# Kernel tuning notes

Measured on AMD Instinct MI355X. Metric: run time of the kernel, lower is better.

## Reference

```python
import jax, jax.numpy as jnp
import numpy as np

R = 2048      # reservoir_size
I = 32        # input_size
O = 32        # output_size
T = 8192      # number of timesteps
SPECTRAL_RADIUS = 0.9


def setup_inputs() -> dict:
    key = jax.random.key(0)
    k1, k2, k3, k4 = jax.random.split(key, 4)
    X = jax.random.normal(k1, (T, I), dtype=jnp.float32)
    # W_in ~ U(-1, 1) as in the torch module
    W_in = jax.random.uniform(k2, (R, I), dtype=jnp.float32, minval=-1.0, maxval=1.0)
    # W_res: random sign-flipped matrix rescaled to target spectral radius.
    # For an iid Gaussian matrix the spectral radius is ~sqrt(R)*std, so
    # scaling by SPECTRAL_RADIUS/sqrt(R) reproduces the rescaling step.
    W_res = jax.random.normal(k3, (R, R), dtype=jnp.float32) * (SPECTRAL_RADIUS / np.sqrt(R))
    W_res = W_res.astype(jnp.float32)
    # W_out: readout over concat([state, input]) -> [O, R + I]
    W_out = jax.random.normal(k4, (O, R + I), dtype=jnp.float32) * 0.02
    state0 = jnp.zeros((R,), dtype=jnp.float32)
    return {"X": X, "W_in": W_in, "W_res": W_res, "W_out": W_out, "state0": state0}


def reference(X, W_in, W_res, W_out, state0):
    """ESN.predict: sequential tanh reservoir recurrence + linear readout.

    state_{t+1} = tanh(W_in @ x_t + W_res @ state_t)
    pred_t      = W_out @ concat([state_{t+1}, x_t])
    Loop runs over the first T-1 inputs (matches `range(X.shape[0]-1)`),
    and since output_size == input_size the torch code returns the T-1
    predictions (initial zero column dropped).
    """
    def step(state, x):  # state: [R], x: [I]
        new_state = jnp.tanh(W_in @ x + W_res @ state)
        pred = W_out @ jnp.concatenate([new_state, x])  # [O]
        return new_state, pred

    _, preds = jax.lax.scan(step, state0, X[:-1])
    return preds  # [T-1, O]
```

## Files before the change

### kernel.cpp

```cpp
#include <hip/hip_runtime.h>
#include <hip/hip_fp16.h>
#include <math.h>


#define R_    2048
#define I_    32
#define O_    32
#define NSTEP 8191
#define G_    256
#define BLK   256
#define TB    4
#define CAPP  (1u << 24)

typedef unsigned int u32;
typedef unsigned long long u64;

__device__ __forceinline__ float tanh_fast(float u) {
    float e = __expf(2.f * u);
    return 1.f - __fdividef(2.f, e + 1.f);
}
__device__ __forceinline__ u32 pkh(float v, u32 tag) {
    return (tag << 16) | (u32)__half_as_ushort(__float2half(v));
}
__device__ __forceinline__ u64 ald(const u64* p) {
    return __hip_atomic_load(p, __ATOMIC_RELAXED, __HIP_MEMORY_SCOPE_AGENT);
}
__device__ __forceinline__ float h2f(u32 b) {
    return __half2float(__ushort_as_half((unsigned short)(b & 0xFFFFu)));
}


__global__ __launch_bounds__(256) void esn_readout(const u32* __restrict__ states,
                                                   const float* __restrict__ W_out,
                                                   const float* __restrict__ X,
                                                   float* __restrict__ out)
{
    __shared__ float s_arr[TB][R_];
    const int t0  = blockIdx.x * TB;
    const int tid = threadIdx.x;
    #pragma unroll
    for (int i = 0; i < TB; ++i) {
        const int t = t0 + i;
        if (t < NSTEP) {
            const u64* p64 = (const u64*)(states + (size_t)(t + 1) * R_);
            #pragma unroll
            for (int q = 0; q < 4; ++q) {
                u64 a = *(const u64*)(&p64[q * 256 + tid]);
                float2 f; f.x = h2f((u32)a); f.y = h2f((u32)(a >> 32));
                *reinterpret_cast<float2*>(&s_arr[i][q * 512 + 2 * tid]) = f;
            }
        }
    }
    __syncthreads();
    const int o = tid >> 3, c = tid & 7;
    const float* wrow = W_out + (size_t)o * (R_ + I_) + c * 256;
    float a0 = 0.f, a1 = 0.f, a2 = 0.f, a3 = 0.f;
    #pragma unroll 8
    for (int j = 0; j < 256; j += 4) {
        float4 wv = *reinterpret_cast<const float4*>(wrow + j);
        float4 s0 = *reinterpret_cast<const float4*>(&s_arr[0][c * 256 + j]);
        float4 s1 = *reinterpret_cast<const float4*>(&s_arr[1][c * 256 + j]);
        float4 s2 = *reinterpret_cast<const float4*>(&s_arr[2][c * 256 + j]);
        float4 s3 = *reinterpret_cast<const float4*>(&s_arr[3][c * 256 + j]);
        a0 = fmaf(wv.x, s0.x, a0); a0 = fmaf(wv.y, s0.y, a0);
        a0 = fmaf(wv.z, s0.z, a0); a0 = fmaf(wv.w, s0.w, a0);
        a1 = fmaf(wv.x, s1.x, a1); a1 = fmaf(wv.y, s1.y, a1);
        a1 = fmaf(wv.z, s1.z, a1); a1 = fmaf(wv.w, s1.w, a1);
        a2 = fmaf(wv.x, s2.x, a2); a2 = fmaf(wv.y, s2.y, a2);
        a2 = fmaf(wv.z, s2.z, a2); a2 = fmaf(wv.w, s2.w, a2);
        a3 = fmaf(wv.x, s3.x, a3); a3 = fmaf(wv.y, s3.y, a3);
        a3 = fmaf(wv.z, s3.z, a3); a3 = fmaf(wv.w, s3.w, a3);
    }
    if (c == 7) {
        const float* wx = W_out + (size_t)o * (R_ + I_) + R_;
        #pragma unroll
        for (int j = 0; j < 32; j += 4) {
            float4 wv = *reinterpret_cast<const float4*>(wx + j);
            float4 x0 = *reinterpret_cast<const float4*>(X + (size_t)(t0 + 0) * I_ + j);
            a0 = fmaf(wv.x, x0.x, a0); a0 = fmaf(wv.y, x0.y, a0);
            a0 = fmaf(wv.z, x0.z, a0); a0 = fmaf(wv.w, x0.w, a0);
            if (t0 + 1 < NSTEP) {
                float4 x1 = *reinterpret_cast<const float4*>(X + (size_t)(t0 + 1) * I_ + j);
                a1 = fmaf(wv.x, x1.x, a1); a1 = fmaf(wv.y, x1.y, a1);
                a1 = fmaf(wv.z, x1.z, a1); a1 = fmaf(wv.w, x1.w, a1);
            }
            if (t0 + 2 < NSTEP) {
                float4 x2 = *reinterpret_cast<const float4*>(X + (size_t)(t0 + 2) * I_ + j);
                a2 = fmaf(wv.x, x2.x, a2); a2 = fmaf(wv.y, x2.y, a2);
                a2 = fmaf(wv.z, x2.z, a2); a2 = fmaf(wv.w, x2.w, a2);
            }
            if (t0 + 3 < NSTEP) {
                float4 x3 = *reinterpret_cast<const float4*>(X + (size_t)(t0 + 3) * I_ + j);
                a3 = fmaf(wv.x, x3.x, a3); a3 = fmaf(wv.y, x3.y, a3);
                a3 = fmaf(wv.z, x3.z, a3); a3 = fmaf(wv.w, x3.w, a3);
            }
        }
    }
    a0 += __shfl_xor(a0, 1, 64); a0 += __shfl_xor(a0, 2, 64); a0 += __shfl_xor(a0, 4, 64);
    a1 += __shfl_xor(a1, 1, 64); a1 += __shfl_xor(a1, 2, 64); a1 += __shfl_xor(a1, 4, 64);
    a2 += __shfl_xor(a2, 1, 64); a2 += __shfl_xor(a2, 2, 64); a2 += __shfl_xor(a2, 4, 64);
    a3 += __shfl_xor(a3, 1, 64); a3 += __shfl_xor(a3, 2, 64); a3 += __shfl_xor(a3, 4, 64);
    if (c == 0) {
        out[(t0 + 0) * O_ + o] = a0;
        if (t0 + 1 < NSTEP) out[(t0 + 1) * O_ + o] = a1;
        if (t0 + 2 < NSTEP) out[(t0 + 2) * O_ + o] = a2;
        if (t0 + 3 < NSTEP) out[(t0 + 3) * O_ + o] = a3;
    }
}

__global__ __launch_bounds__(BLK)
__attribute__((amdgpu_waves_per_eu(1, 1)))
void esn_main(const float* __restrict__ X, const float* __restrict__ W_in,
              const float* __restrict__ W_res, const float* __restrict__ state0,
              u32* __restrict__ ring)
{
    const int tid = threadIdx.x;
    const int g   = blockIdx.x;
    __shared__ float s_lds[2][R_];

    const int lane  = tid & 63;
    const int wave  = tid >> 6;
    const int myrow = g * 8 + wave * 2;

    float w[2][32];
    #pragma unroll
    for (int i = 0; i < 2; ++i) {
        const float* wr = W_res + (size_t)(myrow + i) * R_;
        #pragma unroll
        for (int k = 0; k < 8; ++k) {
            float4 v = *reinterpret_cast<const float4*>(wr + k * 256 + 4 * lane);
            w[i][4*k+0] = v.x; w[i][4*k+1] = v.y;
            w[i][4*k+2] = v.z; w[i][4*k+3] = v.w;
        }
    }
    float wi[2];
    #pragma unroll
    for (int i = 0; i < 2; ++i)
        wi[i] = (lane < 32) ? W_in[(size_t)(myrow + i) * I_ + lane] : 0.f;

    #pragma unroll
    for (int q = 0; q < 8; ++q)
        s_lds[0][q * 256 + tid] = state0[q * 256 + tid];
    __syncthreads();

    float xl = (lane < 32) ? X[lane] : 0.f;

    for (int t = 0; t < NSTEP; ++t) {
        u64 b0 = 0, b1 = 0, b2 = 0, b3 = 0;
        const u64* p64 = (const u64*)(ring + (size_t)(t + 1) * R_);
        if (t < NSTEP - 1) {
            b0 = p64[0 * 256 + tid];
            b1 = p64[1 * 256 + tid];
            b2 = p64[2 * 256 + tid];
            b3 = p64[3 * 256 + tid];
        }

        const float* sbuf = s_lds[t & 1];
        float p0 = wi[0] * xl, p1 = wi[1] * xl;
        #pragma unroll
        for (int k = 0; k < 8; ++k) {
            const float4 sv = *reinterpret_cast<const float4*>(
                &sbuf[k * 256 + 4 * lane]);
            p0 = fmaf(w[0][4*k+0], sv.x, p0); p0 = fmaf(w[0][4*k+1], sv.y, p0);
            p0 = fmaf(w[0][4*k+2], sv.z, p0); p0 = fmaf(w[0][4*k+3], sv.w, p0);
            p1 = fmaf(w[1][4*k+0], sv.x, p1); p1 = fmaf(w[1][4*k+1], sv.y, p1);
            p1 = fmaf(w[1][4*k+2], sv.z, p1); p1 = fmaf(w[1][4*k+3], sv.w, p1);
        }

        float keep = (lane & 1) ? p1 : p0;
        float give = (lane & 1) ? p0 : p1;
        float A = keep + __shfl_xor(give, 1, 64);
        A += __shfl_xor(A, 2, 64);
        A += __shfl_xor(A, 4, 64);
        A += __shfl_xor(A, 8, 64);
        A += __shfl_xor(A, 16, 64);
        A += __shfl_xor(A, 32, 64);

        if (lane < 2) {
            __hip_atomic_store(&ring[(size_t)(t + 1) * R_ + myrow + lane],
                               pkh(tanh_fast(A), (u32)(t + 1)),
                               __ATOMIC_RELAXED, __HIP_MEMORY_SCOPE_AGENT);
        }
        if (t == NSTEP - 1) break;

        float xn = (lane < 32) ? X[(size_t)(t + 1) * I_ + lane] : 0.f;

        u64 a0 = 0, a1 = 0, a2 = 0, a3 = 0;
        {
            const u32 tg  = (u32)(t + 1);
            const u64 pat = ((u64)tg << 48) | ((u64)tg << 16);
            const u64 msk = 0xFFFF0000FFFF0000ull;
            unsigned pend = 0xFu;
            if (!((b0 ^ pat) & msk)) { a0 = b0; pend &= ~1u; }
            if (!((b1 ^ pat) & msk)) { a1 = b1; pend &= ~2u; }
            if (!((b2 ^ pat) & msk)) { a2 = b2; pend &= ~4u; }
            if (!((b3 ^ pat) & msk)) { a3 = b3; pend &= ~8u; }
            unsigned tries = 0;
            while (pend) {
                u64 c0 = 0, c1 = 0, c2 = 0, c3 = 0;
                if (pend & 1u) c0 = ald(&p64[0 * 256 + tid]);
                if (pend & 2u) c1 = ald(&p64[1 * 256 + tid]);
                if (pend & 4u) c2 = ald(&p64[2 * 256 + tid]);
                if (pend & 8u) c3 = ald(&p64[3 * 256 + tid]);
                if ((pend & 1u) && !((c0 ^ pat) & msk)) { a0 = c0; pend &= ~1u; }
                if ((pend & 2u) && !((c1 ^ pat) & msk)) { a1 = c1; pend &= ~2u; }
                if ((pend & 4u) && !((c2 ^ pat) & msk)) { a2 = c2; pend &= ~4u; }
                if ((pend & 8u) && !((c3 ^ pat) & msk)) { a3 = c3; pend &= ~8u; }
                if (!pend) break;
                if (++tries > CAPP) break;
                if (tries > 8) __builtin_amdgcn_s_sleep(1);
            }
        }
        {
            float* dbuf = s_lds[(t + 1) & 1];
            float2 f;
            f.x = h2f((u32)a0); f.y = h2f((u32)(a0 >> 32));
            *reinterpret_cast<float2*>(&dbuf[0 * 512 + 2 * tid]) = f;
            f.x = h2f((u32)a1); f.y = h2f((u32)(a1 >> 32));
            *reinterpret_cast<float2*>(&dbuf[1 * 512 + 2 * tid]) = f;
            f.x = h2f((u32)a2); f.y = h2f((u32)(a2 >> 32));
            *reinterpret_cast<float2*>(&dbuf[2 * 512 + 2 * tid]) = f;
            f.x = h2f((u32)a3); f.y = h2f((u32)(a3 >> 32));
            *reinterpret_cast<float2*>(&dbuf[3 * 512 + 2 * tid]) = f;
        }
        xl = xn;

        asm volatile("s_waitcnt lgkmcnt(0)" ::: "memory");
        __builtin_amdgcn_s_barrier();
        __builtin_amdgcn_sched_barrier(0);
    }
}

extern "C" void kernel_launch(void* const* d_in, const int* in_sizes, int n_in,
                              void* d_out, int out_size, void* d_ws, size_t ws_size,
                              hipStream_t stream)
{
    (void)in_sizes; (void)n_in; (void)out_size; (void)ws_size;
    const float* X      = (const float*)d_in[0];
    const float* W_in   = (const float*)d_in[1];
    const float* W_res  = (const float*)d_in[2];
    const float* W_out  = (const float*)d_in[3];
    const float* state0 = (const float*)d_in[4];
    float* out = (float*)d_out;

    u32* ring = (u32*)((char*)d_ws + 4096);

    hipLaunchKernelGGL(esn_main, dim3(G_), dim3(BLK), 0, stream,
                       X, W_in, W_res, state0, ring);
    hipLaunchKernelGGL(esn_readout, dim3((NSTEP + TB - 1) / TB), dim3(256), 0,
                       stream, ring, W_out, X, out);
}
```

Measured before the change: 8.641 ms.

## Store recurrent weights and state as packed fp16 and use fdot2

Converts the register-resident W_res rows and the LDS state buffer to packed half precision and replaces the fp32 FMA chain with v_dot2_f32_f16 instructions. It also writes the fp16 state received from the ring directly into LDS via byte permutes instead of converting to fp32. This halves the LDS state reads and the FMA count in the per-step matvec, which sits on the serial critical path. The cost is reduced weight precision (fp16 rounding of W_res with round-toward-zero), which may increase numerical error in the recurrence.

```diff
diff --git a/kernel.cpp b/kernel.cpp
--- a/kernel.cpp
+++ b/kernel.cpp
@@ -14,6 +14,7 @@
 
 typedef unsigned int u32;
 typedef unsigned long long u64;
+typedef _Float16 h2v __attribute__((ext_vector_type(2)));
 
 __device__ __forceinline__ float tanh_fast(float u) {
     float e = __expf(2.f * u);
@@ -27,6 +28,14 @@
 }
 __device__ __forceinline__ float h2f(u32 b) {
     return __half2float(__ushort_as_half((unsigned short)(b & 0xFFFFu)));
+}
+__device__ __forceinline__ float fdot2(u32 s, u32 w, float c) {
+    return __builtin_amdgcn_fdot2(__builtin_bit_cast(h2v, s),
+                                  __builtin_bit_cast(h2v, w), c, false);
+}
+__device__ __forceinline__ u32 pkf16(float a, float b) {
+    auto h = __builtin_amdgcn_cvt_pkrtz(a, b);
+    return __builtin_bit_cast(u32, h);
 }
 
 
@@ -116,21 +125,24 @@
 {
     const int tid = threadIdx.x;
     const int g   = blockIdx.x;
-    __shared__ float s_lds[2][R_];
+    __shared__ u32 s16[2][R_ / 2];
 
     const int lane  = tid & 63;
     const int wave  = tid >> 6;
     const int myrow = g * 8 + wave * 2;
 
-    float w[2][32];
+    u32 w16[2][16];
     #pragma unroll
     for (int i = 0; i < 2; ++i) {
         const float* wr = W_res + (size_t)(myrow + i) * R_;
         #pragma unroll
-        for (int k = 0; k < 8; ++k) {
-            float4 v = *reinterpret_cast<const float4*>(wr + k * 256 + 4 * lane);
-            w[i][4*k+0] = v.x; w[i][4*k+1] = v.y;
-            w[i][4*k+2] = v.z; w[i][4*k+3] = v.w;
+        for (int k = 0; k < 4; ++k) {
+            float4 v0 = *reinterpret_cast<const float4*>(wr + k * 512 + 8 * lane);
+            float4 v1 = *reinterpret_cast<const float4*>(wr + k * 512 + 8 * lane + 4);
+            w16[i][4*k+0] = pkf16(v0.x, v0.y);
+            w16[i][4*k+1] = pkf16(v0.z, v0.w);
+            w16[i][4*k+2] = pkf16(v1.x, v1.y);
+            w16[i][4*k+3] = pkf16(v1.z, v1.w);
         }
     }
     float wi[2];
@@ -139,8 +151,10 @@
         wi[i] = (lane < 32) ? W_in[(size_t)(myrow + i) * I_ + lane] : 0.f;
 
     #pragma unroll
-    for (int q = 0; q < 8; ++q)
-        s_lds[0][q * 256 + tid] = state0[q * 256 + tid];
+    for (int q = 0; q < 4; ++q) {
+        const int idx = q * 256 + tid;
+        s16[0][idx] = pkf16(state0[2 * idx], state0[2 * idx + 1]);
+    }
     __syncthreads();
 
     float xl = (lane < 32) ? X[lane] : 0.f;
@@ -155,16 +169,20 @@
             b3 = p64[3 * 256 + tid];
         }
 
-        const float* sbuf = s_lds[t & 1];
+        const u32* sbuf = s16[t & 1];
         float p0 = wi[0] * xl, p1 = wi[1] * xl;
         #pragma unroll
-        for (int k = 0; k < 8; ++k) {
-            const float4 sv = *reinterpret_cast<const float4*>(
+        for (int k = 0; k < 4; ++k) {
+            const uint4 sv = *reinterpret_cast<const uint4*>(
                 &sbuf[k * 256 + 4 * lane]);
-            p0 = fmaf(w[0][4*k+0], sv.x, p0); p0 = fmaf(w[0][4*k+1], sv.y, p0);
-            p0 = fmaf(w[0][4*k+2], sv.z, p0); p0 = fmaf(w[0][4*k+3], sv.w, p0);
-            p1 = fmaf(w[1][4*k+0], sv.x, p1); p1 = fmaf(w[1][4*k+1], sv.y, p1);
-            p1 = fmaf(w[1][4*k+2], sv.z, p1); p1 = fmaf(w[1][4*k+3], sv.w, p1);
+            p0 = fdot2(sv.x, w16[0][4*k+0], p0);
+            p0 = fdot2(sv.y, w16[0][4*k+1], p0);
+            p0 = fdot2(sv.z, w16[0][4*k+2], p0);
+            p0 = fdot2(sv.w, w16[0][4*k+3], p0);
+            p1 = fdot2(sv.x, w16[1][4*k+0], p1);
+            p1 = fdot2(sv.y, w16[1][4*k+1], p1);
+            p1 = fdot2(sv.z, w16[1][4*k+2], p1);
+            p1 = fdot2(sv.w, w16[1][4*k+3], p1);
         }
 
         float keep = (lane & 1) ? p1 : p0;
@@ -212,16 +230,15 @@
             }
         }
         {
-            float* dbuf = s_lds[(t + 1) & 1];
-            float2 f;
-            f.x = h2f((u32)a0); f.y = h2f((u32)(a0 >> 32));
-            *reinterpret_cast<float2*>(&dbuf[0 * 512 + 2 * tid]) = f;
-            f.x = h2f((u32)a1); f.y = h2f((u32)(a1 >> 32));
-            *reinterpret_cast<float2*>(&dbuf[1 * 512 + 2 * tid]) = f;
-            f.x = h2f((u32)a2); f.y = h2f((u32)(a2 >> 32));
-            *reinterpret_cast<float2*>(&dbuf[2 * 512 + 2 * tid]) = f;
-            f.x = h2f((u32)a3); f.y = h2f((u32)(a3 >> 32));
-            *reinterpret_cast<float2*>(&dbuf[3 * 512 + 2 * tid]) = f;
+            u32* dbuf = s16[(t + 1) & 1];
+            dbuf[0 * 256 + tid] =
+                __builtin_amdgcn_perm((u32)(a0 >> 32), (u32)a0, 0x05040100u);
+            dbuf[1 * 256 + tid] =
+                __builtin_amdgcn_perm((u32)(a1 >> 32), (u32)a1, 0x05040100u);
+            dbuf[2 * 256 + tid] =
+                __builtin_amdgcn_perm((u32)(a2 >> 32), (u32)a2, 0x05040100u);
+            dbuf[3 * 256 + tid] =
+                __builtin_amdgcn_perm((u32)(a3 >> 32), (u32)a3, 0x05040100u);
         }
         xl = xn;
 
```

New measurement: 24.56 ms. 2.84x slower.
